# Optimization experiments

Measured on AMD Instinct MI355X. Metric: run time of the kernel, lower is better.

Reference implementation:

```python
import jax, jax.numpy as jnp
import numpy as np

B, N, D, H, C = 8, 1024, 1024, 8, 1
S = 32            # sqrt(D // C): per-patch spatial map side
HD = D // H       # head dim = 128
SCALE = HD ** -0.5
BN_EPS = 1e-3     # Keras BatchNormalization default epsilon


def setup_inputs() -> dict:
    key = jax.random.key(0)
    ks = jax.random.split(key, 7)
    std = 0.02  # matches tf.random_normal_initializer(0.0, 0.02)
    return {
        "x": jax.random.normal(ks[0], (B, N, D), jnp.float32),
        "qw": jax.random.normal(ks[1], (3, 3, C, C), jnp.float32) * std,
        "kw": jax.random.normal(ks[2], (3, 3, C, C), jnp.float32) * std,
        "vw": jax.random.normal(ks[3], (3, 3, C, C), jnp.float32) * std,
        "reatten_w": jax.random.normal(ks[4], (N, N), jnp.float32) / np.float32(np.sqrt(N)),
        "reatten_b": jnp.zeros((N,), jnp.float32),
        "bn_gamma": jnp.ones((N,), jnp.float32),
        "bn_beta": jnp.zeros((N,), jnp.float32),
        "proj_w": jax.random.normal(ks[5], (D, D), jnp.float32) / np.float32(np.sqrt(D)),
        "proj_b": jnp.zeros((D,), jnp.float32),
    }


def _conv_qkv(x, w):
    # unflatten: [B, N, D] -> [B*N, S, S, C]; map_fn over batch with a shared
    # conv == one conv with B*N as batch dim. 3x3 SAME, no bias, exact GELU.
    xm = x.reshape(B * N, S, S, C)
    y = jax.lax.conv_general_dilated(
        xm, w, window_strides=(1, 1), padding='SAME',
        dimension_numbers=('NHWC', 'HWIO', 'NHWC'))
    y = jax.nn.gelu(y, approximate=False)
    # reshape to heads: [B, N, H, HD] -> [B, H, N, HD]
    return y.reshape(B, N, H, HD).transpose(0, 2, 1, 3)


def reference(x, qw, kw, vw, reatten_w, reatten_b, bn_gamma, bn_beta, proj_w, proj_b):
    q = _conv_qkv(x, qw)
    k = _conv_qkv(x, kw)
    v = _conv_qkv(x, vw)

    attn = jax.nn.softmax(jnp.einsum('bhid,bhjd->bhij', q, k) * SCALE, axis=-1)
    # re-attention: 1x1 conv over last (key) axis + BN (inference: mean=0, var=1)
    attn = jnp.einsum('bhic,cj->bhij', attn, reatten_w) + reatten_b
    attn = attn * (bn_gamma / jnp.sqrt(jnp.float32(1.0) + BN_EPS)) + bn_beta
    # reatten_scale = 1.0 (transform_scale=False)

    out = jnp.einsum('bhij,bhjd->bhid', attn, v)
    out = out.transpose(0, 2, 1, 3).reshape(B, N, D)
    out = out @ proj_w + proj_b
    return (out, attn)
```

## Files before the change

### kernel.cpp

```cpp
#include <hip/hip_runtime.h>
#include <hip/hip_bf16.h>

typedef __attribute__((ext_vector_type(8))) short short8;
typedef __attribute__((ext_vector_type(4))) float f32x4;

__device__ __forceinline__ void gload_lds16(const void* g, void* l) {
    __builtin_amdgcn_global_load_lds(
        (const __attribute__((address_space(1))) void*)g,
        (__attribute__((address_space(3))) void*)l, 16, 0, 0);
}

__device__ __forceinline__ float gelu_exact(float x) {
    return 0.5f * x * (1.0f + erff(x * 0.70710678118654752f));
}
__device__ __forceinline__ float us2f(unsigned int u) {
    return __uint_as_float(u << 16);
}
__device__ __forceinline__ unsigned short f2b_raw(float f) {
    __hip_bfloat16 h = __float2bfloat16(f);
    return *reinterpret_cast<unsigned short*>(&h);
}
__device__ __forceinline__ float tofloat(float f) { return f; }
__device__ __forceinline__ float tofloat(__hip_bfloat16 h) { return __bfloat162float(h); }

__global__ __launch_bounds__(256) void conv_qkv(
    const float* __restrict__ x,
    const float* __restrict__ qw, const float* __restrict__ kw, const float* __restrict__ vw,
    __hip_bfloat16* __restrict__ qb, __hip_bfloat16* __restrict__ kb, __hip_bfloat16* __restrict__ vb)
{
    __shared__ float img[1024];
    const int bid = blockIdx.x;
    const int b = bid >> 10, n = bid & 1023;
    const float* xr = x + (long)bid * 1024;
    for (int i = threadIdx.x; i < 1024; i += 256) img[i] = xr[i];
    __syncthreads();

    float wq[9], wk[9], wv[9];
    #pragma unroll
    for (int i = 0; i < 9; ++i) { wq[i] = qw[i]; wk[i] = kw[i]; wv[i] = vw[i]; }

    for (int q = 0; q < 4; ++q) {
        const int p = q * 256 + threadIdx.x;
        const int r = p >> 5, c = p & 31;
        float sq = 0.f, sk = 0.f, sv = 0.f;
        #pragma unroll
        for (int dy = 0; dy < 3; ++dy) {
            const int rr = r + dy - 1;
            if (rr < 0 || rr > 31) continue;
            #pragma unroll
            for (int dx = 0; dx < 3; ++dx) {
                const int cc = c + dx - 1;
                if (cc < 0 || cc > 31) continue;
                const float px = img[rr * 32 + cc];
                sq += px * wq[dy * 3 + dx];
                sk += px * wk[dy * 3 + dx];
                sv += px * wv[dy * 3 + dx];
            }
        }
        sq = gelu_exact(sq); sk = gelu_exact(sk); sv = gelu_exact(sv);
        const int h = p >> 7, d = p & 127;
        const long off = ((long)(b * 8 + h) * 1024 + n) * 128 + d;
        qb[off] = __float2bfloat16(sq);
        kb[off] = __float2bfloat16(sk);
        vb[off] = __float2bfloat16(sv);
    }
}

template <typename Tin>
__global__ __launch_bounds__(256) void transpose_cast(
    const Tin* __restrict__ in, __hip_bfloat16* __restrict__ out,
    int R, int Cc, long inz, long outz)
{
    __shared__ float tile[32][33];
    const long z = blockIdx.z;
    const int c0 = blockIdx.x * 32, r0 = blockIdx.y * 32;
    const int tx = threadIdx.x & 31, ty = threadIdx.x >> 5;
    const Tin* ip = in + z * inz;
    #pragma unroll
    for (int i = 0; i < 32; i += 8)
        tile[ty + i][tx] = tofloat(ip[(long)(r0 + ty + i) * Cc + (c0 + tx)]);
    __syncthreads();
    __hip_bfloat16* op = out + z * outz;
    #pragma unroll
    for (int i = 0; i < 32; i += 8)
        op[(long)(c0 + ty + i) * R + (r0 + tx)] = __float2bfloat16(tile[tx][ty + i]);
}

__global__ __launch_bounds__(256) void softmax_inplace(__hip_bfloat16* __restrict__ S)
{
    __shared__ float red[8];
    const long row = blockIdx.x;
    uint2* p = reinterpret_cast<uint2*>(S + row * 1024);
    const int tid = threadIdx.x;
    uint2 u = p[tid];
    float v0 = us2f(u.x & 0xffffu), v1 = us2f(u.x >> 16);
    float v2 = us2f(u.y & 0xffffu), v3 = us2f(u.y >> 16);

    float m = fmaxf(fmaxf(v0, v1), fmaxf(v2, v3));
    for (int o = 32; o; o >>= 1) m = fmaxf(m, __shfl_xor(m, o));
    const int wave = tid >> 6, lane = tid & 63;
    if (lane == 0) red[wave] = m;
    __syncthreads();
    m = fmaxf(fmaxf(red[0], red[1]), fmaxf(red[2], red[3]));

    float e0 = expf(v0 - m), e1 = expf(v1 - m), e2 = expf(v2 - m), e3 = expf(v3 - m);
    float s = e0 + e1 + e2 + e3;
    for (int o = 32; o; o >>= 1) s += __shfl_xor(s, o);
    if (lane == 0) red[4 + wave] = s;
    __syncthreads();
    s = red[4] + red[5] + red[6] + red[7];
    const float inv = 1.0f / s;

    u.x = (unsigned int)f2b_raw(e0 * inv) | ((unsigned int)f2b_raw(e1 * inv) << 16);
    u.y = (unsigned int)f2b_raw(e2 * inv) | ((unsigned int)f2b_raw(e3 * inv) << 16);
    p[tid] = u;
}

template <int MODE>
__global__ __launch_bounds__(256) void gemm_nt(
    const void* __restrict__ Aall, const __hip_bfloat16* __restrict__ Ball,
    void* __restrict__ Call, int K,
    long sAz, long sBz, long sCz,
    const float* __restrict__ e0, const float* __restrict__ e1, const float* __restrict__ e2)
{
    constexpr bool AF32 = (MODE == 2);
    constexpr bool OF32 = (MODE == 1 || MODE == 3);

    __shared__ __align__(16) char smem[32 * 132 * 4];
    short* As = (short*)smem;
    short* Bs = (short*)(smem + 8192);
    float* cbuf = (float*)smem;

    const int tid = threadIdx.x;
    const int z = blockIdx.z;
    const int tileM = blockIdx.x, tileN = blockIdx.y;

    const short* AwB = nullptr;
    const float* AwF = nullptr;
    if constexpr (AF32) AwF = (const float*)Aall + sAz * z + (long)tileM * 128 * K;
    else                AwB = (const short*)Aall + sAz * z + (long)tileM * 128 * K;
    const short* Bw = (const short*)Ball + sBz * z + (long)tileN * 128 * K;

    const int r0s = tid >> 2, k0s = (tid & 3) * 8;
    const int r1s = r0s + 64;

    f32x4 acc[4][4];
    #pragma unroll
    for (int m = 0; m < 4; ++m)
        #pragma unroll
        for (int n = 0; n < 4; ++n) acc[m][n] = (f32x4){0.f, 0.f, 0.f, 0.f};

    const int lane = tid & 63;
    const int wave = tid >> 6;
    const int wr = (wave >> 1) * 64, wc = (wave & 1) * 64;
    const int fr = lane & 15;
    const int kb = (lane >> 4) * 8;

    const int nk = K >> 5;
    for (int kt = 0; kt < nk; ++kt) {
        if constexpr (AF32) {
            const float* Ak0 = AwF + (long)r0s * K + kt * 32 + k0s;
            const float* Ak1 = AwF + (long)r1s * K + kt * 32 + k0s;
            f32x4 a00 = *(const f32x4*)Ak0;
            f32x4 a01 = *(const f32x4*)(Ak0 + 4);
            f32x4 a10 = *(const f32x4*)Ak1;
            f32x4 a11 = *(const f32x4*)(Ak1 + 4);
            __syncthreads();
            short8 s0, s1;
            #pragma unroll
            for (int i = 0; i < 4; ++i) {
                s0[i] = (short)f2b_raw(a00[i]); s0[i + 4] = (short)f2b_raw(a01[i]);
                s1[i] = (short)f2b_raw(a10[i]); s1[i + 4] = (short)f2b_raw(a11[i]);
            }
            *(short8*)&As[tid * 8] = s0;
            *(short8*)&As[(tid + 256) * 8] = s1;
            gload_lds16(Bw + (long)r0s * K + kt * 32 + k0s, &Bs[tid * 8]);
            gload_lds16(Bw + (long)r1s * K + kt * 32 + k0s, &Bs[(tid + 256) * 8]);
            __syncthreads();
        } else {
            __syncthreads();
            gload_lds16(AwB + (long)r0s * K + kt * 32 + k0s, &As[tid * 8]);
            gload_lds16(AwB + (long)r1s * K + kt * 32 + k0s, &As[(tid + 256) * 8]);
            gload_lds16(Bw + (long)r0s * K + kt * 32 + k0s, &Bs[tid * 8]);
            gload_lds16(Bw + (long)r1s * K + kt * 32 + k0s, &Bs[(tid + 256) * 8]);
            __syncthreads();
        }

        short8 af[4], bf[4];
        #pragma unroll
        for (int m = 0; m < 4; ++m) af[m] = *(const short8*)&As[(wr + m * 16 + fr) * 32 + kb];
        #pragma unroll
        for (int n = 0; n < 4; ++n) bf[n] = *(const short8*)&Bs[(wc + n * 16 + fr) * 32 + kb];
        #pragma unroll
        for (int m = 0; m < 4; ++m)
            #pragma unroll
            for (int n = 0; n < 4; ++n)
                acc[m][n] = __builtin_amdgcn_mfma_f32_16x16x32_bf16(af[m], bf[n], acc[m][n], 0, 0, 0);
    }

    long cbase;
    if (MODE == 2) cbase = (long)(z >> 3) * 1048576 + (long)(z & 7) * 128;
    else           cbase = sCz * z;

    float alpha[4], addv[4];
    #pragma unroll
    for (int n = 0; n < 4; ++n) {
        const int col = tileN * 128 + wc + n * 16 + fr;
        float a_ = 1.f, b_ = 0.f;
        if (MODE == 0) a_ = 0.08838834764831843f;
        if (MODE == 1) {
            const float g = e0[col], rbv = e1[col], bt = e2[col];
            a_ = g * rsqrtf(1.0f + 1e-3f);
            b_ = rbv * a_ + bt;
        }
        if (MODE == 3) b_ = e0[col];
        alpha[n] = a_; addv[n] = b_;
    }

    __syncthreads();
    #pragma unroll
    for (int q = 0; q < 4; ++q) {
        if ((wave >> 1) == (q >> 1)) {
            #pragma unroll
            for (int mm = 0; mm < 2; ++mm) {
                const int m = (q & 1) * 2 + mm;
                const int lr0 = m * 16 + (lane >> 4) * 4 - (q & 1) * 32;
                #pragma unroll
                for (int n = 0; n < 4; ++n)
                    #pragma unroll
                    for (int r = 0; r < 4; ++r)
                        cbuf[(lr0 + r) * 132 + wc + n * 16 + fr] = acc[m][n][r] * alpha[n] + addv[n];
            }
        }
        __syncthreads();
        const long growbase = (long)tileM * 128 + q * 32;
        if constexpr (OF32) {
            float* Cg = (float*)Call + cbase;
            #pragma unroll
            for (int pass = 0; pass < 4; ++pass) {
                const int idx = (tid + pass * 256) * 4;
                const int row = idx >> 7, col = idx & 127;
                f32x4 v = *(const f32x4*)&cbuf[row * 132 + col];
                *(f32x4*)&Cg[(growbase + row) * 1024 + tileN * 128 + col] = v;
            }
        } else {
            __hip_bfloat16* Cg = (__hip_bfloat16*)Call + cbase;
            #pragma unroll
            for (int pass = 0; pass < 2; ++pass) {
                const int idx = (tid + pass * 256) * 8;
                const int row = idx >> 7, col = idx & 127;
                const float* src = &cbuf[row * 132 + col];
                f32x4 v0 = *(const f32x4*)src;
                f32x4 v1 = *(const f32x4*)(src + 4);
                short8 s;
                #pragma unroll
                for (int i = 0; i < 4; ++i) {
                    s[i] = (short)f2b_raw(v0[i]);
                    s[i + 4] = (short)f2b_raw(v1[i]);
                }
                *(short8*)&Cg[(growbase + row) * 1024 + tileN * 128 + col] = s;
            }
        }
        __syncthreads();
    }
}

extern "C" void kernel_launch(void* const* d_in, const int* in_sizes, int n_in,
                              void* d_out, int out_size, void* d_ws, size_t ws_size,
                              hipStream_t stream)
{
    const float* x  = (const float*)d_in[0];
    const float* qw = (const float*)d_in[1];
    const float* kw = (const float*)d_in[2];
    const float* vw = (const float*)d_in[3];
    const float* rw = (const float*)d_in[4];
    const float* rb = (const float*)d_in[5];
    const float* bg = (const float*)d_in[6];
    const float* bb = (const float*)d_in[7];
    const float* pw = (const float*)d_in[8];
    const float* pb = (const float*)d_in[9];

    float* outF  = (float*)d_out;
    float* attnF = outF + 8388608;

    char* w = (char*)d_ws;
    __hip_bfloat16* qb    = (__hip_bfloat16*)w; w += 16777216;
    __hip_bfloat16* kb    = (__hip_bfloat16*)w; w += 16777216;
    __hip_bfloat16* vb    = (__hip_bfloat16*)w; w += 16777216;
    __hip_bfloat16* vt    = (__hip_bfloat16*)w; w += 16777216;
    __hip_bfloat16* Wt    = (__hip_bfloat16*)w; w += 2097152;
    __hip_bfloat16* pWt   = (__hip_bfloat16*)w; w += 2097152;
    __hip_bfloat16* o2    = (__hip_bfloat16*)w; w += 16777216;
    __hip_bfloat16* S     = (__hip_bfloat16*)w; w += 134217728;

    conv_qkv<<<8192, 256, 0, stream>>>(x, qw, kw, vw, qb, kb, vb);
    transpose_cast<float><<<dim3(32, 32, 1), 256, 0, stream>>>(rw, Wt, 1024, 1024, 0, 0);
    transpose_cast<float><<<dim3(32, 32, 1), 256, 0, stream>>>(pw, pWt, 1024, 1024, 0, 0);
    transpose_cast<__hip_bfloat16><<<dim3(4, 32, 64), 256, 0, stream>>>(vb, vt, 1024, 128, 131072, 131072);

    gemm_nt<0><<<dim3(8, 8, 64), 256, 0, stream>>>(
        qb, kb, S, 128, 131072, 131072, 1048576, nullptr, nullptr, nullptr);
    softmax_inplace<<<65536, 256, 0, stream>>>(S);
    gemm_nt<1><<<dim3(8, 8, 64), 256, 0, stream>>>(
        S, Wt, attnF, 1024, 1048576, 0, 1048576, bg, rb, bb);
    gemm_nt<2><<<dim3(8, 1, 64), 256, 0, stream>>>(
        attnF, vt, o2, 1024, 1048576, 131072, 0, nullptr, nullptr, nullptr);
    gemm_nt<3><<<dim3(64, 8, 1), 256, 0, stream>>>(
        o2, pWt, outF, 1024, 0, 0, 0, pb, nullptr, nullptr);
}
```

Before: 460.9 us.

## Add dedicated 256x256-tile pipelined GEMM for the re-attention matmul

Replaces the generic 128x128 gemm_nt MODE 1 for the large re-attention GEMM (64 batches of 1024x1024x1024) with a 512-thread kernel using 256x256 output tiles. It stages four LDS buffers with direct global-to-LDS loads, XOR-swizzles the LDS layout to avoid bank conflicts, interleaves MFMA with prefetch under explicit barriers and raised priority, and keeps the BN-affine epilogue. The larger tile roughly doubles operand reuse and should cut global/LDS traffic per flop. In exchange it uses 128KB of LDS and many accumulator registers, which limits occupancy, and the hand-written waitcnt schedule must be exactly right to stay correct.

New measurement: 423.8 us. 1.09x faster.

```diff
diff --git a/kernel.cpp b/kernel.cpp
--- a/kernel.cpp
+++ b/kernel.cpp
@@ -9,6 +9,8 @@
         (const __attribute__((address_space(1))) void*)g,
         (__attribute__((address_space(3))) void*)l, 16, 0, 0);
 }
+
+#define SBAR() do { __builtin_amdgcn_sched_barrier(0); __builtin_amdgcn_s_barrier(); __builtin_amdgcn_sched_barrier(0); } while (0)
 
 __device__ __forceinline__ float gelu_exact(float x) {
     return 0.5f * x * (1.0f + erff(x * 0.70710678118654752f));
@@ -116,15 +118,144 @@
     p[tid] = u;
 }
 
+__global__ __launch_bounds__(512, 2) void gemm_reatten_256(
+    const __hip_bfloat16* __restrict__ Sall, const __hip_bfloat16* __restrict__ Wt,
+    float* __restrict__ Cout,
+    const float* __restrict__ bg, const float* __restrict__ rb, const float* __restrict__ bb)
+{
+    __shared__ __align__(16) char smem[131072];
+    char* ldsA = smem;
+    char* ldsB = smem + 65536;
+
+    const int tid = threadIdx.x;
+    const int z = blockIdx.z, tileM = blockIdx.x, tileN = blockIdx.y;
+    const char* Ab = (const char*)(Sall + (long)z * 1048576 + (long)tileM * 256 * 1024);
+    const char* Bb = (const char*)(Wt + (long)tileN * 256 * 1024);
+
+    int grow[2], goff[2], pphys[2];
+    #pragma unroll
+    for (int i = 0; i < 2; ++i) {
+        const int p = i * 8192 + tid * 16;
+        const int l = p ^ (((p >> 7) & 3) << 4);
+        pphys[i] = p; grow[i] = l >> 6; goff[i] = l & 63;
+    }
+    auto STAGE = [&](const char* gb, char* lb, int kt) {
+        #pragma unroll
+        for (int i = 0; i < 2; ++i)
+            gload_lds16(gb + (long)grow[i] * 2048 + kt * 64 + goff[i], lb + pphys[i]);
+    };
+
+    const int lane = tid & 63, wid = tid >> 6;
+    const int wrM = wid >> 2, wcn = wid & 3;
+    const int fr = lane & 15, kl = lane >> 4;
+    const int frbase = fr * 64 + kl * 16;
+
+    auto LD8 = [&](const char* buf, int L) -> short8 {
+        const int ph = L ^ (((L >> 7) & 3) << 4);
+        return *(const short8*)(buf + ph);
+    };
+
+    f32x4 acc[8][4];
+    #pragma unroll
+    for (int m = 0; m < 8; ++m)
+        #pragma unroll
+        for (int n = 0; n < 4; ++n) acc[m][n] = (f32x4){0.f, 0.f, 0.f, 0.f};
+
+    STAGE(Ab, ldsA, 0);          STAGE(Bb, ldsB, 0);
+    STAGE(Ab, ldsA + 16384, 1);  STAGE(Bb, ldsB + 16384, 1);
+    asm volatile("s_waitcnt vmcnt(4)" ::: "memory");
+    SBAR();
+
+    #pragma unroll 1
+    for (int t = 0; t < 32; ++t) {
+        char* bufA = ldsA + (t & 3) * 16384;
+        char* bufB = ldsB + (t & 3) * 16384;
+        const int t2 = t + 2;
+        char* nA = ldsA + (t2 & 3) * 16384;
+        char* nB = ldsB + (t2 & 3) * 16384;
+
+        short8 bf[4], af[4];
+        #pragma unroll
+        for (int n = 0; n < 4; ++n) bf[n] = LD8(bufB, ((wcn * 64 + n * 16) * 64) + frbase);
+        #pragma unroll
+        for (int j = 0; j < 4; ++j) af[j] = LD8(bufA, ((wrM * 128 + j * 16) * 64) + frbase);
+        if (t2 < 32) STAGE(Ab, nA, t2);
+        SBAR();
+        asm volatile("s_waitcnt lgkmcnt(0)" ::: "memory");
+        __builtin_amdgcn_sched_barrier(0);
+        __builtin_amdgcn_s_setprio(1);
+        #pragma unroll
+        for (int j = 0; j < 4; ++j)
+            #pragma unroll
+            for (int n = 0; n < 4; ++n)
+                acc[j][n] = __builtin_amdgcn_mfma_f32_16x16x32_bf16(af[j], bf[n], acc[j][n], 0, 0, 0);
+        __builtin_amdgcn_s_setprio(0);
+        SBAR();
+
+        #pragma unroll
+        for (int j = 0; j < 4; ++j) af[j] = LD8(bufA, ((wrM * 128 + 64 + j * 16) * 64) + frbase);
+        if (t2 < 32) STAGE(Bb, nB, t2);
+        SBAR();
+        asm volatile("s_waitcnt lgkmcnt(0)" ::: "memory");
+        __builtin_amdgcn_sched_barrier(0);
+        __builtin_amdgcn_s_setprio(1);
+        #pragma unroll
+        for (int j = 0; j < 4; ++j)
+            #pragma unroll
+            for (int n = 0; n < 4; ++n)
+                acc[4 + j][n] = __builtin_amdgcn_mfma_f32_16x16x32_bf16(af[j], bf[n], acc[4 + j][n], 0, 0, 0);
+        __builtin_amdgcn_s_setprio(0);
+        if (t < 30)       asm volatile("s_waitcnt vmcnt(4)" ::: "memory");
+        else if (t == 30) asm volatile("s_waitcnt vmcnt(0)" ::: "memory");
+        SBAR();
+    }
+
+    __syncthreads();
+    float* cbuf = (float*)smem;
+    const float bninv = rsqrtf(1.0f + 1e-3f);
+    float alpha[4], addv[4];
+    #pragma unroll
+    for (int n = 0; n < 4; ++n) {
+        const int col = tileN * 256 + wcn * 64 + n * 16 + fr;
+        const float g = bg[col];
+        alpha[n] = g * bninv;
+        addv[n] = rb[col] * alpha[n] + bb[col];
+    }
+    const int srow = tid >> 3, cseg = (tid & 7) * 4;
+    #pragma unroll
+    for (int c = 0; c < 4; ++c) {
+        if (wrM == (c >> 1)) {
+            #pragma unroll
+            for (int j = 0; j < 4; ++j) {
+                const int mf = (c & 1) * 4 + j;
+                const int lrow0 = j * 16 + kl * 4;
+                #pragma unroll
+                for (int n = 0; n < 4; ++n)
+                    #pragma unroll
+                    for (int r = 0; r < 4; ++r)
+                        cbuf[(lrow0 + r) * 260 + wcn * 64 + n * 16 + fr] =
+                            acc[mf][n][r] * alpha[n] + addv[n];
+            }
+        }
+        __syncthreads();
+        float* gptr = Cout + (long)z * 1048576 +
+                      (long)(tileM * 256 + c * 64 + srow) * 1024 + tileN * 256;
+        #pragma unroll
+        for (int i = 0; i < 8; ++i)
+            *(f32x4*)(gptr + cseg + i * 32) = *(const f32x4*)&cbuf[srow * 260 + cseg + i * 32];
+        __syncthreads();
+    }
+}
+
 template <int MODE>
 __global__ __launch_bounds__(256) void gemm_nt(
     const void* __restrict__ Aall, const __hip_bfloat16* __restrict__ Ball,
     void* __restrict__ Call, int K,
     long sAz, long sBz, long sCz,
-    const float* __restrict__ e0, const float* __restrict__ e1, const float* __restrict__ e2)
+    const float* __restrict__ e0)
 {
     constexpr bool AF32 = (MODE == 2);
-    constexpr bool OF32 = (MODE == 1 || MODE == 3);
+    constexpr bool OF32 = (MODE == 3);
 
     __shared__ __align__(16) char smem[32 * 132 * 4];
     short* As = (short*)smem;
@@ -208,11 +339,6 @@
         const int col = tileN * 128 + wc + n * 16 + fr;
         float a_ = 1.f, b_ = 0.f;
         if (MODE == 0) a_ = 0.08838834764831843f;
-        if (MODE == 1) {
-            const float g = e0[col], rbv = e1[col], bt = e2[col];
-            a_ = g * rsqrtf(1.0f + 1e-3f);
-            b_ = rbv * a_ + bt;
-        }
         if (MODE == 3) b_ = e0[col];
         alpha[n] = a_; addv[n] = b_;
     }
@@ -299,12 +425,11 @@
     transpose_cast<__hip_bfloat16><<<dim3(4, 32, 64), 256, 0, stream>>>(vb, vt, 1024, 128, 131072, 131072);
 
     gemm_nt<0><<<dim3(8, 8, 64), 256, 0, stream>>>(
-        qb, kb, S, 128, 131072, 131072, 1048576, nullptr, nullptr, nullptr);
+        qb, kb, S, 128, 131072, 131072, 1048576, nullptr);
     softmax_inplace<<<65536, 256, 0, stream>>>(S);
-    gemm_nt<1><<<dim3(8, 8, 64), 256, 0, stream>>>(
-        S, Wt, attnF, 1024, 1048576, 0, 1048576, bg, rb, bb);
+    gemm_reatten_256<<<dim3(4, 4, 64), 512, 0, stream>>>(S, Wt, attnF, bg, rb, bb);
     gemm_nt<2><<<dim3(8, 1, 64), 256, 0, stream>>>(
-        attnF, vt, o2, 1024, 1048576, 131072, 0, nullptr, nullptr, nullptr);
+        attnF, vt, o2, 1024, 1048576, 131072, 0, nullptr);
     gemm_nt<3><<<dim3(64, 8, 1), 256, 0, stream>>>(
-        o2, pWt, outF, 1024, 0, 0, 0, pb, nullptr, nullptr);
-}
+        o2, pWt, outF, 1024, 0, 0, 0, pb);
+}
```
